# Kernel tuning notes

Measured on AMD Instinct MI355X. Metric: run time of the kernel, lower is better.

## Reference

```python
import jax, jax.numpy as jnp
from jax import lax
import numpy as np

SIGMA = 5.0
ALPHA = 50.0
RADIUS = int(4.0 * SIGMA + 0.5)  # scipy gaussian_filter truncate=4.0 -> 20


def _gauss_kernel():
    t = jnp.arange(-RADIUS, RADIUS + 1, dtype=jnp.float32)
    phi = jnp.exp(-0.5 * (t / SIGMA) ** 2)
    return phi / phi.sum()


def _gaussian_blur(f):
    # f: [B, H, W]. scipy mode='reflect' (edge included) == jnp.pad mode='symmetric'.
    k = _gauss_kernel()
    K = 2 * RADIUS + 1
    fp = jnp.pad(f, ((0, 0), (RADIUS, RADIUS), (RADIUS, RADIUS)), mode='symmetric')[:, None]
    z = lax.conv_general_dilated(fp, k.reshape(1, 1, K, 1), (1, 1), 'VALID')
    z = lax.conv_general_dilated(z, k.reshape(1, 1, 1, K), (1, 1), 'VALID')
    return z[:, 0]


def _reflect(i, n):
    # scipy mode='reflect': (d c b a | a b c d | d c b a), period 2n on integer indices
    i = jnp.mod(i, 2 * n)
    return jnp.where(i >= n, 2 * n - 1 - i, i)


def _bilinear(img, yy, xx):
    # img: [H, W]; yy/xx: [H, W] float sample coords (rows, cols)
    H, W = img.shape
    y0 = jnp.floor(yy)
    x0 = jnp.floor(xx)
    wy = yy - y0
    wx = xx - x0
    y0i = y0.astype(jnp.int32)
    x0i = x0.astype(jnp.int32)
    y0r = _reflect(y0i, H)
    y1r = _reflect(y0i + 1, H)
    x0r = _reflect(x0i, W)
    x1r = _reflect(x0i + 1, W)
    v00 = img[y0r, x0r]
    v01 = img[y0r, x1r]
    v10 = img[y1r, x0r]
    v11 = img[y1r, x1r]
    return (v00 * (1 - wy) * (1 - wx) + v01 * (1 - wy) * wx
            + v10 * wy * (1 - wx) + v11 * wy * wx)


def setup_inputs() -> dict:
    key = jax.random.key(0)
    k1, k2, k3 = jax.random.split(key, 3)
    B, H, W = 64, 512, 512
    x = jax.random.normal(k1, (B, 1, H, W), dtype=jnp.float32)
    rand_dx = jax.random.uniform(k2, (B, H, W), dtype=jnp.float32)
    rand_dy = jax.random.uniform(k3, (B, H, W), dtype=jnp.float32)
    return {"x": x, "rand_dx": rand_dx, "rand_dy": rand_dy}


def reference(x, rand_dx, rand_dy):
    # x: [B, 1, H, W]
    B, C, H, W = x.shape
    dx = _gaussian_blur(rand_dx * 2.0 - 1.0) * ALPHA  # [B, H, W]
    dy = _gaussian_blur(rand_dy * 2.0 - 1.0) * ALPHA
    gx, gy = jnp.meshgrid(jnp.arange(W, dtype=x.dtype), jnp.arange(H, dtype=x.dtype))
    yy = gy[None] + dy  # row coords
    xx = gx[None] + dx  # col coords
    warped = jax.vmap(_bilinear)(x[:, 0], yy, xx)  # [B, H, W]
    return warped[:, None]
```

## Files before the change

### kernel.cpp

```cpp
#include <hip/hip_runtime.h>

#define RADIUS 20
#define KSIZE  41
#define ALPHA_F 50.0f
#define TY     8
#define WID    512
#define HEI    512
#define PW     (WID + 2 * RADIUS)
#define NRQ    44
#define PF     8

typedef float floatx4 __attribute__((ext_vector_type(4)));

__device__ constexpr float G[KSIZE] = {
    2.6770e-05f, 5.8390e-05f, 1.22380e-04f, 2.46460e-04f, 4.76840e-04f,
    8.86410e-04f, 1.583160e-03f, 2.716710e-03f, 4.479090e-03f, 7.095210e-03f,
    1.0798630e-02f, 1.5790680e-02f, 2.2185070e-02f, 2.9946720e-02f, 3.8838800e-02f,
    4.8396120e-02f, 5.7940680e-02f, 6.6647650e-02f, 7.3657040e-02f, 7.8211730e-02f,
    7.9791720e-02f,
    7.8211730e-02f, 7.3657040e-02f, 6.6647650e-02f, 5.7940680e-02f, 4.8396120e-02f,
    3.8838800e-02f, 2.9946720e-02f, 2.2185070e-02f, 1.5790680e-02f, 1.0798630e-02f,
    7.095210e-03f, 4.479090e-03f, 2.716710e-03f, 1.583160e-03f, 8.86410e-04f,
    4.76840e-04f, 2.46460e-04f, 1.22380e-04f, 5.8390e-05f, 2.6770e-05f
};

__device__ __forceinline__ int refl(int i, int n) {
    i = (i < 0) ? (-1 - i) : i;
    i = (i >= n) ? (2 * n - 1 - i) : i;
    return i;
}

__device__ __forceinline__ int refl512(int i) {
    i = (i < 0) ? (-1 - i) : i;
    return (i >= 512) ? (1023 - i) : i;
}

template<bool INTERIOR>
__device__ __forceinline__ void vblur4(const float* __restrict__ src, int ybase,
                                       float acc[4][4]) {
    float ring[PF][4];
    #pragma unroll
    for (int k = 0; k < PF; ++k) {
        const int gy = INTERIOR ? (ybase + k) : refl(ybase + k, HEI);
        const float4 v = *reinterpret_cast<const float4*>(src + (size_t)gy * WID);
        ring[k][0] = v.x; ring[k][1] = v.y; ring[k][2] = v.z; ring[k][3] = v.w;
    }
    #pragma unroll
    for (int r = 0; r < NRQ; ++r) {
        float v[4];
        #pragma unroll
        for (int j = 0; j < 4; ++j) v[j] = ring[r & (PF - 1)][j];
        if (r + PF < NRQ) {
            const int gy = INTERIOR ? (ybase + r + PF) : refl(ybase + r + PF, HEI);
            const float4 nv = *reinterpret_cast<const float4*>(src + (size_t)gy * WID);
            ring[r & (PF - 1)][0] = nv.x; ring[r & (PF - 1)][1] = nv.y;
            ring[r & (PF - 1)][2] = nv.z; ring[r & (PF - 1)][3] = nv.w;
        }
        #pragma unroll
        for (int o = 0; o < 4; ++o) {
            const int t = r - o;
            if (t >= 0 && t < KSIZE) {
                const float g = G[t];
                #pragma unroll
                for (int j = 0; j < 4; ++j) acc[o][j] = fmaf(g, v[j], acc[o][j]);
            }
        }
    }
}

__global__ __launch_bounds__(512, 4) void elastic_kernel(
    const float* __restrict__ xin, const float* __restrict__ rdx,
    const float* __restrict__ rdy, float* __restrict__ outp, int B) {

    __shared__ float sdx[TY][PW];
    __shared__ float sdy[TY][PW];

    const int tid = threadIdx.x;

    int b, band;
    {
        const int L = blockIdx.x;
        if (B == 64) {
            const int xcd = L & 7;
            const int s   = L >> 3;
            b    = xcd * 8 + (s >> 6);
            band = s & 63;
        } else {
            b    = L / (HEI / TY);
            band = L % (HEI / TY);
        }
    }
    const int y0 = band * TY;
    const size_t base = (size_t)b * (HEI * WID);

    {
        const int c4 = tid & 127;
        const int f  = (tid >> 7) & 1;
        const int rq = tid >> 8;
        const int ybase = y0 + 4 * rq - RADIUS;

        const float* src = (f ? rdy : rdx) + base + 4 * c4;
        float (*sd)[PW] = f ? sdy : sdx;

        float acc[4][4];
        #pragma unroll
        for (int o = 0; o < 4; ++o)
            #pragma unroll
            for (int j = 0; j < 4; ++j) acc[o][j] = 0.f;

        if (ybase >= 0 && ybase + NRQ <= HEI) vblur4<true >(src, ybase, acc);
        else                                  vblur4<false>(src, ybase, acc);

        #pragma unroll
        for (int o = 0; o < 4; ++o) {
            const int row = 4 * rq + o;
            float sv[4];
            #pragma unroll
            for (int j = 0; j < 4; ++j) sv[j] = 2.f * acc[o][j] - 1.f;
            float4 pack;
            pack.x = sv[0]; pack.y = sv[1]; pack.z = sv[2]; pack.w = sv[3];
            *reinterpret_cast<float4*>(&sd[row][RADIUS + 4 * c4]) = pack;
            if (c4 < 5) {
                #pragma unroll
                for (int j = 0; j < 4; ++j) sd[row][RADIUS - 1 - (4 * c4 + j)] = sv[j];
            }
            if (c4 >= 123) {
                #pragma unroll
                for (int j = 0; j < 4; ++j) sd[row][RADIUS + 2 * WID - 1 - (4 * c4 + j)] = sv[j];
            }
        }
    }
    __syncthreads();

    const int c4 = tid & 127;
    const int rg = tid >> 7;
    const float* img = xin + base;

    #pragma unroll
    for (int i = 0; i < 2; ++i) {
        const int o  = rg + 4 * i;
        const int gy = y0 + o;

        float dxv[4] = {0.f, 0.f, 0.f, 0.f};
        float dyv[4] = {0.f, 0.f, 0.f, 0.f};

        const float4* rpx = (const float4*)(&sdx[o][0]);
        const float4* rpy = (const float4*)(&sdy[o][0]);
        #pragma unroll
        for (int q = 0; q < 11; ++q) {
            const float4 vx = rpx[c4 + q];
            const float4 vy = rpy[c4 + q];
            const float ex[4] = {vx.x, vx.y, vx.z, vx.w};
            const float ey[4] = {vy.x, vy.y, vy.z, vy.w};
            #pragma unroll
            for (int e = 0; e < 4; ++e) {
                const int k = 4 * q + e;
                #pragma unroll
                for (int j = 0; j < 4; ++j) {
                    const int t = k - j;
                    if (t >= 0 && t < KSIZE) {
                        const float g = G[t];
                        dxv[j] = fmaf(g, ex[e], dxv[j]);
                        dyv[j] = fmaf(g, ey[e], dyv[j]);
                    }
                }
            }
        }

        float st[4];
        #pragma unroll
        for (int j = 0; j < 4; ++j) {
            const int col = 4 * c4 + j;
            float xx = (float)col + dxv[j] * ALPHA_F;
            float yy = (float)gy  + dyv[j] * ALPHA_F;
            xx = fminf(fmaxf(xx, -511.f), 1022.f);
            yy = fminf(fmaxf(yy, -511.f), 1022.f);
            const float x0f = floorf(xx), y0f = floorf(yy);
            const float wx = xx - x0f, wy = yy - y0f;
            const int x0 = (int)x0f, yb = (int)y0f;
            const int x0r = refl512(x0);
            const int x1r = refl512(x0 + 1);
            const int y0r = refl512(yb);
            const int y1r = refl512(yb + 1);

            const float* r0 = img + ((size_t)y0r << 9);
            const float* r1 = img + ((size_t)y1r << 9);
            const float v00 = r0[x0r];
            const float v01 = r0[x1r];
            const float v10 = r1[x0r];
            const float v11 = r1[x1r];

            const float top = fmaf(wx, v01 - v00, v00);
            const float bot = fmaf(wx, v11 - v10, v10);
            st[j] = fmaf(wy, bot - top, top);
        }

        floatx4 pack;
        pack.x = st[0]; pack.y = st[1]; pack.z = st[2]; pack.w = st[3];
        __builtin_nontemporal_store(pack,
            reinterpret_cast<floatx4*>(outp + base + (size_t)gy * WID + 4 * c4));
    }
}

extern "C" void kernel_launch(void* const* d_in, const int* in_sizes, int n_in,
                              void* d_out, int out_size, void* d_ws, size_t ws_size,
                              hipStream_t stream) {
    const float* x   = (const float*)d_in[0];
    const float* rdx = (const float*)d_in[1];
    const float* rdy = (const float*)d_in[2];
    float* out = (float*)d_out;

    const int B = in_sizes[1] / (HEI * WID);

    const int nblocks = B * (HEI / TY);
    elastic_kernel<<<nblocks, 512, 0, stream>>>(x, rdx, rdy, out, B);
    (void)d_ws; (void)ws_size; (void)n_in; (void)out_size;
}
```

Baseline: 294.0 us.

## Split fused kernel into separate vertical-blur and warp kernels via workspace

Splits the fused kernel into two launches. The first computes the vertical Gaussian blur for 16-row bands, with 8 output rows per thread, and writes the reflect-padded result to a global workspace. The second reads that buffer to do the horizontal blur and bilinear warp. This cuts the halo re-reading overhead of the vertical blur (48 rows read per 16 output rows instead of 44 per 8). In exchange it adds a full round trip of the intermediate through global memory plus a second launch. The old fused kernel remains as a fallback when the workspace is missing or too small.

```diff
diff --git a/kernel.cpp b/kernel.cpp
--- a/kernel.cpp
+++ b/kernel.cpp
@@ -8,6 +8,7 @@
 #define HEI    512
 #define PW     (WID + 2 * RADIUS)
 #define NRQ    44
+#define NRH    48
 #define PF     8
 
 typedef float floatx4 __attribute__((ext_vector_type(4)));
@@ -68,12 +69,103 @@
     }
 }
 
-__global__ __launch_bounds__(512, 4) void elastic_kernel(
-    const float* __restrict__ xin, const float* __restrict__ rdx,
-    const float* __restrict__ rdy, float* __restrict__ outp, int B) {
-
-    __shared__ float sdx[TY][PW];
-    __shared__ float sdy[TY][PW];
+template<bool INTERIOR>
+__device__ __forceinline__ void vblur8(const float* __restrict__ src, int ybase,
+                                       float acc[8][4]) {
+    float ring[PF][4];
+    #pragma unroll
+    for (int k = 0; k < PF; ++k) {
+        const int gy = INTERIOR ? (ybase + k) : refl(ybase + k, HEI);
+        const float4 v = *reinterpret_cast<const float4*>(src + (size_t)gy * WID);
+        ring[k][0] = v.x; ring[k][1] = v.y; ring[k][2] = v.z; ring[k][3] = v.w;
+    }
+    #pragma unroll
+    for (int r = 0; r < NRH; ++r) {
+        float v[4];
+        #pragma unroll
+        for (int j = 0; j < 4; ++j) v[j] = ring[r & (PF - 1)][j];
+        if (r + PF < NRH) {
+            const int gy = INTERIOR ? (ybase + r + PF) : refl(ybase + r + PF, HEI);
+            const float4 nv = *reinterpret_cast<const float4*>(src + (size_t)gy * WID);
+            ring[r & (PF - 1)][0] = nv.x; ring[r & (PF - 1)][1] = nv.y;
+            ring[r & (PF - 1)][2] = nv.z; ring[r & (PF - 1)][3] = nv.w;
+        }
+        #pragma unroll
+        for (int o = 0; o < 8; ++o) {
+            const int t = r - o;
+            if (t >= 0 && t < KSIZE) {
+                const float g = G[t];
+                #pragma unroll
+                for (int j = 0; j < 4; ++j) acc[o][j] = fmaf(g, v[j], acc[o][j]);
+            }
+        }
+    }
+}
+
+__global__ __launch_bounds__(512) void vblur_kernel(
+    const float* __restrict__ rdx, const float* __restrict__ rdy,
+    float* __restrict__ vd, int B) {
+
+    const int tid = threadIdx.x;
+
+    int b, band;
+    {
+        const int L = blockIdx.x;
+        if (B == 64) {
+            const int xcd = L & 7;
+            const int s   = L >> 3;
+            b    = xcd * 8 + (s >> 5);
+            band = s & 31;
+        } else {
+            b    = L / (HEI / 16);
+            band = L % (HEI / 16);
+        }
+    }
+    const int y0 = band * 16;
+    const size_t base = (size_t)b * (HEI * WID);
+    const size_t fstride = (size_t)B * HEI * PW;
+
+    const int c4 = tid & 127;
+    const int f  = (tid >> 7) & 1;
+    const int h  = tid >> 8;
+    const int ybase = y0 + 8 * h - RADIUS;
+
+    const float* src = (f ? rdy : rdx) + base + 4 * c4;
+    float* dst = vd + (size_t)f * fstride + (size_t)b * HEI * PW;
+
+    float acc[8][4];
+    #pragma unroll
+    for (int o = 0; o < 8; ++o)
+        #pragma unroll
+        for (int j = 0; j < 4; ++j) acc[o][j] = 0.f;
+
+    if (ybase >= 0 && ybase + NRH <= HEI) vblur8<true >(src, ybase, acc);
+    else                                  vblur8<false>(src, ybase, acc);
+
+    #pragma unroll
+    for (int o = 0; o < 8; ++o) {
+        const int row = y0 + 8 * h + o;
+        float* rp = dst + (size_t)row * PW;
+        float sv[4];
+        #pragma unroll
+        for (int j = 0; j < 4; ++j) sv[j] = 2.f * acc[o][j] - 1.f;
+        float4 pack;
+        pack.x = sv[0]; pack.y = sv[1]; pack.z = sv[2]; pack.w = sv[3];
+        *reinterpret_cast<float4*>(rp + RADIUS + 4 * c4) = pack;
+        if (c4 < 5) {
+            #pragma unroll
+            for (int j = 0; j < 4; ++j) rp[RADIUS - 1 - (4 * c4 + j)] = sv[j];
+        }
+        if (c4 >= 123) {
+            #pragma unroll
+            for (int j = 0; j < 4; ++j) rp[RADIUS + 2 * WID - 1 - (4 * c4 + j)] = sv[j];
+        }
+    }
+}
+
+__global__ __launch_bounds__(512) void warp_kernel(
+    const float* __restrict__ xin, const float* __restrict__ vd,
+    float* __restrict__ outp, int B) {
 
     const int tid = threadIdx.x;
 
@@ -92,60 +184,24 @@
     }
     const int y0 = band * TY;
     const size_t base = (size_t)b * (HEI * WID);
-
-    {
-        const int c4 = tid & 127;
-        const int f  = (tid >> 7) & 1;
-        const int rq = tid >> 8;
-        const int ybase = y0 + 4 * rq - RADIUS;
-
-        const float* src = (f ? rdy : rdx) + base + 4 * c4;
-        float (*sd)[PW] = f ? sdy : sdx;
-
-        float acc[4][4];
-        #pragma unroll
-        for (int o = 0; o < 4; ++o)
-            #pragma unroll
-            for (int j = 0; j < 4; ++j) acc[o][j] = 0.f;
-
-        if (ybase >= 0 && ybase + NRQ <= HEI) vblur4<true >(src, ybase, acc);
-        else                                  vblur4<false>(src, ybase, acc);
-
-        #pragma unroll
-        for (int o = 0; o < 4; ++o) {
-            const int row = 4 * rq + o;
-            float sv[4];
-            #pragma unroll
-            for (int j = 0; j < 4; ++j) sv[j] = 2.f * acc[o][j] - 1.f;
-            float4 pack;
-            pack.x = sv[0]; pack.y = sv[1]; pack.z = sv[2]; pack.w = sv[3];
-            *reinterpret_cast<float4*>(&sd[row][RADIUS + 4 * c4]) = pack;
-            if (c4 < 5) {
-                #pragma unroll
-                for (int j = 0; j < 4; ++j) sd[row][RADIUS - 1 - (4 * c4 + j)] = sv[j];
-            }
-            if (c4 >= 123) {
-                #pragma unroll
-                for (int j = 0; j < 4; ++j) sd[row][RADIUS + 2 * WID - 1 - (4 * c4 + j)] = sv[j];
-            }
-        }
-    }
-    __syncthreads();
+    const size_t fstride = (size_t)B * HEI * PW;
 
     const int c4 = tid & 127;
     const int rg = tid >> 7;
     const float* img = xin + base;
+    const float* vbase = vd + (size_t)b * HEI * PW;
 
     #pragma unroll
     for (int i = 0; i < 2; ++i) {
         const int o  = rg + 4 * i;
         const int gy = y0 + o;
 
+        const float4* rpx = (const float4*)(vbase + (size_t)gy * PW);
+        const float4* rpy = (const float4*)(vbase + fstride + (size_t)gy * PW);
+
         float dxv[4] = {0.f, 0.f, 0.f, 0.f};
         float dyv[4] = {0.f, 0.f, 0.f, 0.f};
 
-        const float4* rpx = (const float4*)(&sdx[o][0]);
-        const float4* rpy = (const float4*)(&sdy[o][0]);
         #pragma unroll
         for (int q = 0; q < 11; ++q) {
             const float4 vx = rpx[c4 + q];
@@ -202,6 +258,140 @@
     }
 }
 
+__global__ __launch_bounds__(512, 4) void elastic_kernel(
+    const float* __restrict__ xin, const float* __restrict__ rdx,
+    const float* __restrict__ rdy, float* __restrict__ outp, int B) {
+
+    __shared__ float sdx[TY][PW];
+    __shared__ float sdy[TY][PW];
+
+    const int tid = threadIdx.x;
+
+    int b, band;
+    {
+        const int L = blockIdx.x;
+        if (B == 64) {
+            const int xcd = L & 7;
+            const int s   = L >> 3;
+            b    = xcd * 8 + (s >> 6);
+            band = s & 63;
+        } else {
+            b    = L / (HEI / TY);
+            band = L % (HEI / TY);
+        }
+    }
+    const int y0 = band * TY;
+    const size_t base = (size_t)b * (HEI * WID);
+
+    {
+        const int c4 = tid & 127;
+        const int f  = (tid >> 7) & 1;
+        const int rq = tid >> 8;
+        const int ybase = y0 + 4 * rq - RADIUS;
+
+        const float* src = (f ? rdy : rdx) + base + 4 * c4;
+        float (*sd)[PW] = f ? sdy : sdx;
+
+        float acc[4][4];
+        #pragma unroll
+        for (int o = 0; o < 4; ++o)
+            #pragma unroll
+            for (int j = 0; j < 4; ++j) acc[o][j] = 0.f;
+
+        if (ybase >= 0 && ybase + NRQ <= HEI) vblur4<true >(src, ybase, acc);
+        else                                  vblur4<false>(src, ybase, acc);
+
+        #pragma unroll
+        for (int o = 0; o < 4; ++o) {
+            const int row = 4 * rq + o;
+            float sv[4];
+            #pragma unroll
+            for (int j = 0; j < 4; ++j) sv[j] = 2.f * acc[o][j] - 1.f;
+            float4 pack;
+            pack.x = sv[0]; pack.y = sv[1]; pack.z = sv[2]; pack.w = sv[3];
+            *reinterpret_cast<float4*>(&sd[row][RADIUS + 4 * c4]) = pack;
+            if (c4 < 5) {
+                #pragma unroll
+                for (int j = 0; j < 4; ++j) sd[row][RADIUS - 1 - (4 * c4 + j)] = sv[j];
+            }
+            if (c4 >= 123) {
+                #pragma unroll
+                for (int j = 0; j < 4; ++j) sd[row][RADIUS + 2 * WID - 1 - (4 * c4 + j)] = sv[j];
+            }
+        }
+    }
+    __syncthreads();
+
+    const int c4 = tid & 127;
+    const int rg = tid >> 7;
+    const float* img = xin + base;
+
+    #pragma unroll
+    for (int i = 0; i < 2; ++i) {
+        const int o  = rg + 4 * i;
+        const int gy = y0 + o;
+
+        float dxv[4] = {0.f, 0.f, 0.f, 0.f};
+        float dyv[4] = {0.f, 0.f, 0.f, 0.f};
+
+        const float4* rpx = (const float4*)(&sdx[o][0]);
+        const float4* rpy = (const float4*)(&sdy[o][0]);
+        #pragma unroll
+        for (int q = 0; q < 11; ++q) {
+            const float4 vx = rpx[c4 + q];
+            const float4 vy = rpy[c4 + q];
+            const float ex[4] = {vx.x, vx.y, vx.z, vx.w};
+            const float ey[4] = {vy.x, vy.y, vy.z, vy.w};
+            #pragma unroll
+            for (int e = 0; e < 4; ++e) {
+                const int k = 4 * q + e;
+                #pragma unroll
+                for (int j = 0; j < 4; ++j) {
+                    const int t = k - j;
+                    if (t >= 0 && t < KSIZE) {
+                        const float g = G[t];
+                        dxv[j] = fmaf(g, ex[e], dxv[j]);
+                        dyv[j] = fmaf(g, ey[e], dyv[j]);
+                    }
+                }
+            }
+        }
+
+        float st[4];
+        #pragma unroll
+        for (int j = 0; j < 4; ++j) {
+            const int col = 4 * c4 + j;
+            float xx = (float)col + dxv[j] * ALPHA_F;
+            float yy = (float)gy  + dyv[j] * ALPHA_F;
+            xx = fminf(fmaxf(xx, -511.f), 1022.f);
+            yy = fminf(fmaxf(yy, -511.f), 1022.f);
+            const float x0f = floorf(xx), y0f = floorf(yy);
+            const float wx = xx - x0f, wy = yy - y0f;
+            const int x0 = (int)x0f, yb = (int)y0f;
+            const int x0r = refl512(x0);
+            const int x1r = refl512(x0 + 1);
+            const int y0r = refl512(yb);
+            const int y1r = refl512(yb + 1);
+
+            const float* r0 = img + ((size_t)y0r << 9);
+            const float* r1 = img + ((size_t)y1r << 9);
+            const float v00 = r0[x0r];
+            const float v01 = r0[x1r];
+            const float v10 = r1[x0r];
+            const float v11 = r1[x1r];
+
+            const float top = fmaf(wx, v01 - v00, v00);
+            const float bot = fmaf(wx, v11 - v10, v10);
+            st[j] = fmaf(wy, bot - top, top);
+        }
+
+        floatx4 pack;
+        pack.x = st[0]; pack.y = st[1]; pack.z = st[2]; pack.w = st[3];
+        __builtin_nontemporal_store(pack,
+            reinterpret_cast<floatx4*>(outp + base + (size_t)gy * WID + 4 * c4));
+    }
+}
+
 extern "C" void kernel_launch(void* const* d_in, const int* in_sizes, int n_in,
                               void* d_out, int out_size, void* d_ws, size_t ws_size,
                               hipStream_t stream) {
@@ -212,7 +402,12 @@
 
     const int B = in_sizes[1] / (HEI * WID);
 
-    const int nblocks = B * (HEI / TY);
-    elastic_kernel<<<nblocks, 512, 0, stream>>>(x, rdx, rdy, out, B);
-    (void)d_ws; (void)ws_size; (void)n_in; (void)out_size;
-}
+    const size_t need = (size_t)2 * B * HEI * PW * sizeof(float);
+    if (d_ws != nullptr && ws_size >= need) {
+        vblur_kernel<<<B * (HEI / 16), 512, 0, stream>>>(rdx, rdy, (float*)d_ws, B);
+        warp_kernel <<<B * (HEI / TY), 512, 0, stream>>>(x, (const float*)d_ws, out, B);
+    } else {
+        elastic_kernel<<<B * (HEI / TY), 512, 0, stream>>>(x, rdx, rdy, out, B);
+    }
+    (void)n_in; (void)out_size;
+}
```

New measurement: 355.1 us. 1.21x slower.
